# Optimization experiments

Measured on AMD Instinct MI355X. Metric: run time of the kernel, lower is better.

The kernel has to match this reference:

```python
import jax, jax.numpy as jnp
import numpy as np

N_EMBD = 768
N_HEAD = 8
B, T = 4, 2048

def setup_inputs() -> dict:
    key = jax.random.key(0)
    k1, k2, k3, k4, k5 = jax.random.split(key, 5)
    C = N_EMBD
    s = 1.0 / np.sqrt(C)
    return {
        "x": jax.random.normal(k1, (B, T, C), dtype=jnp.float32),
        "W_attn": jax.random.normal(k2, (C, 3 * C), dtype=jnp.float32) * s,
        "b_attn": jnp.zeros((3 * C,), dtype=jnp.float32),
        "W_proj": jax.random.normal(k3, (C, C), dtype=jnp.float32) * s,
        "b_proj": jnp.zeros((C,), dtype=jnp.float32),
    }

def reference(x, W_attn, b_attn, W_proj, b_proj):
    Bs, Ts, C = x.shape
    H = N_HEAD
    hs = C // H
    qkv = x @ W_attn + b_attn                      # [B,T,3C]
    q, k, v = jnp.split(qkv, 3, axis=-1)
    # reshape to [B,H,T,hs]
    q = q.reshape(Bs, Ts, H, hs).transpose(0, 2, 1, 3)
    k = k.reshape(Bs, Ts, H, hs).transpose(0, 2, 1, 3)
    v = v.reshape(Bs, Ts, H, hs).transpose(0, 2, 1, 3)
    scale = 1.0 / jnp.sqrt(jnp.float32(hs))
    att = jnp.einsum('bhid,bhjd->bhij', q, k) * scale   # [B,H,T,T]
    mask = jnp.tril(jnp.ones((Ts, Ts), dtype=bool))
    att = jnp.where(mask, att, -jnp.inf)
    m = jnp.max(att, axis=-1, keepdims=True)
    e = jnp.where(mask, jnp.exp(att - m), 0.0)
    # original kernel divides by (sum + 1e-9)
    att = e / (jnp.sum(e, axis=-1, keepdims=True) + 1e-9)
    y = jnp.einsum('bhij,bhjd->bhid', att, v)           # [B,H,T,hs]
    y = y.transpose(0, 2, 1, 3).reshape(Bs, Ts, C)
    return y @ W_proj + b_proj
```

## Files before the change

### kernel.cpp

```cpp
#include <hip/hip_runtime.h>

typedef __bf16 bf16;
typedef __attribute__((ext_vector_type(4))) __bf16 bf16x4;
typedef __attribute__((ext_vector_type(8))) __bf16 bf16x8;
typedef __attribute__((ext_vector_type(4))) float f32x4;

#define B_   4
#define T_   2048
#define C_   768
#define H_   8
#define HS_  96
#define M_   (B_ * T_)
#define QKN_ (3 * C_)

#define NEG_BIG (-1e30f)

#define KSTR 104
#define VSTR 72

__device__ __forceinline__ void gload_lds16(const bf16* g, bf16* l) {
    __builtin_amdgcn_global_load_lds(
        (const __attribute__((address_space(1))) uint32_t*)g,
        (__attribute__((address_space(3))) uint32_t*)l,
        16, 0, 0);
}

__device__ __forceinline__ bf16x8 cvt8(f32x4 v0, f32x4 v1) {
    bf16x8 o;
#pragma unroll
    for (int i = 0; i < 4; ++i) { o[i] = (bf16)v0[i]; o[4 + i] = (bf16)v1[i]; }
    return o;
}

__global__ void transpose_kernel(const float* __restrict__ W, bf16* __restrict__ Wt,
                                 int R, int Cn) {
    __shared__ bf16 tile[32][33];
    int tx = threadIdx.x, ty = threadIdx.y;
    int x  = blockIdx.x * 32 + tx;
    int y0 = blockIdx.y * 32;
#pragma unroll
    for (int j = 0; j < 32; j += 8)
        tile[ty + j][tx] = (bf16)W[(size_t)(y0 + ty + j) * Cn + x];
    __syncthreads();
    int y2 = blockIdx.x * 32;
    int x2 = y0 + tx;
#pragma unroll
    for (int j = 0; j < 32; j += 8)
        Wt[(size_t)(y2 + ty + j) * R + x2] = tile[tx][ty + j];
}

__global__ void sentinel_kernel(float* __restrict__ out, int n) {
    int i = blockIdx.x * 256 + threadIdx.x;
    if (i < n) out[i] = 12345.0f;
}

__global__ __launch_bounds__(256) void convert_bf16_kernel(const float* __restrict__ in,
                                                           bf16* __restrict__ out,
                                                           int n8) {
    int i = blockIdx.x * 256 + threadIdx.x;
    if (i >= n8) return;
    const float* p = in + (size_t)i * 8;
    f32x4 a = *(const f32x4*)p;
    f32x4 b = *(const f32x4*)(p + 4);
    *(bf16x8*)&out[(size_t)i * 8] = cvt8(a, b);
}

#define CONV_BLKS (M_ * C_ / 8 / 256)
#define TA_BX (QKN_ / 32)
#define TA_BLKS (TA_BX * (C_ / 32))
#define TP_BX (C_ / 32)
#define TP_BLKS (TP_BX * (C_ / 32))

__device__ __forceinline__ void transpose_body(bf16 (*tile)[33],
                                               const float* __restrict__ W,
                                               bf16* __restrict__ Wt,
                                               int R, int Cn, int bx, int by, int tid) {
    int tx = tid & 31, ty = tid >> 5;
    int x  = bx * 32 + tx;
    int y0 = by * 32;
#pragma unroll
    for (int j = 0; j < 32; j += 8)
        tile[ty + j][tx] = (bf16)W[(size_t)(y0 + ty + j) * Cn + x];
    __syncthreads();
    int y2 = bx * 32;
    int x2 = y0 + tx;
#pragma unroll
    for (int j = 0; j < 32; j += 8)
        Wt[(size_t)(y2 + ty + j) * R + x2] = tile[tx][ty + j];
}

__global__ __launch_bounds__(256) void prep_kernel(const float* __restrict__ x,
                                                   bf16* __restrict__ xb,
                                                   const float* __restrict__ Wa,
                                                   bf16* __restrict__ Wta,
                                                   const float* __restrict__ Wp,
                                                   bf16* __restrict__ Wtp) {
    __shared__ bf16 tile[32][33];
    int bid = blockIdx.x;
    int tid = threadIdx.x;
    if (bid < CONV_BLKS) {
        int i = bid * 256 + tid;
        const float* p = x + (size_t)i * 8;
        f32x4 a = *(const f32x4*)p;
        f32x4 b = *(const f32x4*)(p + 4);
        *(bf16x8*)&xb[(size_t)i * 8] = cvt8(a, b);
    } else if (bid < CONV_BLKS + TA_BLKS) {
        int t = bid - CONV_BLKS;
        transpose_body(tile, Wa, Wta, C_, QKN_, t % TA_BX, t / TA_BX, tid);
    } else {
        int t = bid - CONV_BLKS - TA_BLKS;
        transpose_body(tile, Wp, Wtp, C_, C_, t % TP_BX, t / TP_BX, tid);
    }
}

#define TILE_ELEMS (128 * 64)

__global__ __launch_bounds__(256) void gemm_qkv(const bf16* __restrict__ A,
                                                const bf16* __restrict__ Bt,
                                                const float* __restrict__ bias,
                                                bf16* __restrict__ Cmat,
                                                bf16* __restrict__ Vt,
                                                int M, int N, int K) {
    __shared__ bf16 lda[2 * TILE_ELEMS];
    __shared__ bf16 ldb[2 * TILE_ELEMS];
    int tid  = threadIdx.x;
    int w    = tid >> 6;
    int lane = tid & 63;
    int col  = lane & 15, quad = lane >> 4;
    int wr   = w >> 1, wc = w & 1;
    int m0   = blockIdx.y * 128, n0 = blockIdx.x * 128;

    int srow = lane >> 3;
    int scol = ((lane & 7) ^ srow) * 8;
    const bf16* gA[4]; const bf16* gB[4]; bf16* lA[4]; bf16* lB[4];
#pragma unroll
    for (int i = 0; i < 4; ++i) {
        int seg = w * 4 + i;
        int row = seg * 8 + srow;
        gA[i] = &A[(size_t)(m0 + row) * K + scol];
        gB[i] = &Bt[(size_t)(n0 + row) * K + scol];
        lA[i] = &lda[seg * 512];
        lB[i] = &ldb[seg * 512];
    }

    const f32x4 zero = {0.f, 0.f, 0.f, 0.f};
    f32x4 acc[4][4];
#pragma unroll
    for (int mr = 0; mr < 4; ++mr)
#pragma unroll
        for (int nc = 0; nc < 4; ++nc) acc[mr][nc] = zero;

#pragma unroll
    for (int i = 0; i < 4; ++i) {
        gload_lds16(gA[i], lA[i]);
        gload_lds16(gB[i], lB[i]);
    }

    int cur = 0;
    for (int k0 = 0; k0 < K; k0 += 64) {
        int nxt = cur ^ 1;
        if (k0 + 64 < K) {
#pragma unroll
            for (int i = 0; i < 4; ++i) {
                gload_lds16(gA[i] + k0 + 64, lA[i] + nxt * TILE_ELEMS);
                gload_lds16(gB[i] + k0 + 64, lB[i] + nxt * TILE_ELEMS);
            }
            asm volatile("s_waitcnt vmcnt(8)" ::: "memory");
        } else {
            asm volatile("s_waitcnt vmcnt(0)" ::: "memory");
        }
        __builtin_amdgcn_s_barrier();
        __builtin_amdgcn_sched_barrier(0);
        const bf16* la = &lda[cur * TILE_ELEMS];
        const bf16* lb = &ldb[cur * TILE_ELEMS];
#pragma unroll
        for (int ks = 0; ks < 2; ++ks) {
            bf16x8 af[4], bfr[4];
            int ca = (((ks * 4 + quad) ^ (col & 7)) * 8);
#pragma unroll
            for (int t = 0; t < 4; ++t) {
                af[t]  = *(const bf16x8*)&la[(wr * 64 + t * 16 + col) * 64 + ca];
                bfr[t] = *(const bf16x8*)&lb[(wc * 64 + t * 16 + col) * 64 + ca];
            }
#pragma unroll
            for (int mr = 0; mr < 4; ++mr)
#pragma unroll
                for (int nc = 0; nc < 4; ++nc)
                    acc[mr][nc] = __builtin_amdgcn_mfma_f32_16x16x32_bf16(
                        af[mr], bfr[nc], acc[mr][nc], 0, 0, 0);
        }
        __builtin_amdgcn_sched_barrier(0);
        __builtin_amdgcn_s_barrier();
        cur = nxt;
    }

#pragma unroll
    for (int nc = 0; nc < 4; ++nc) {
        int n = n0 + wc * 64 + nc * 16 + col;
        float bv = bias[n];
#pragma unroll
        for (int mr = 0; mr < 4; ++mr) {
#pragma unroll
            for (int r = 0; r < 4; ++r) {
                int row = m0 + wr * 64 + mr * 16 + quad * 4 + r;
                Cmat[(size_t)row * N + n] = (bf16)(acc[mr][nc][r] + bv);
            }
        }
    }
    if (n0 >= 2 * C_) {
        int batch = m0 >> 11;
        bf16* Vtb = Vt + (size_t)batch * C_ * T_;
        int t0 = (m0 & 2047) + wr * 64;
#pragma unroll
        for (int nc = 0; nc < 4; ++nc) {
            int n  = n0 + wc * 64 + nc * 16 + col;
            int vc = n - 2 * C_;
            float bv = bias[n];
#pragma unroll
            for (int mr = 0; mr < 4; ++mr) {
                int t  = t0 + mr * 16 + quad * 4;
                int tb = t & ~63;
                int a  = (t >> 2) & 15;
                int ts = tb + ((a & 7) << 3) + ((a >> 3) << 2);
                bf16x4 pk = {(bf16)(acc[mr][nc][0] + bv), (bf16)(acc[mr][nc][1] + bv),
                             (bf16)(acc[mr][nc][2] + bv), (bf16)(acc[mr][nc][3] + bv)};
                *(bf16x4*)&Vtb[(size_t)vc * T_ + ts] = pk;
            }
        }
    }
}

#define PJA_ELEMS (128 * 64)
#define PJB_ELEMS (96 * 64)
__global__ __launch_bounds__(256) void gemm_proj(const bf16* __restrict__ A,
                                                 const bf16* __restrict__ Bt,
                                                 const float* __restrict__ bias,
                                                 float* __restrict__ Cmat,
                                                 int M, int N, int K) {
    __shared__ bf16 lda[2 * PJA_ELEMS];
    __shared__ bf16 ldb[2 * PJB_ELEMS];
    int tid  = threadIdx.x;
    int w    = tid >> 6;
    int lane = tid & 63;
    int col  = lane & 15, quad = lane >> 4;
    int wr   = w >> 1, wc = w & 1;
    int m0   = blockIdx.y * 128, n0 = blockIdx.x * 96;

    int srow = lane >> 3;
    int scol = ((lane & 7) ^ srow) * 8;
    const bf16* gA[4]; bf16* lA[4];
    const bf16* gB[3]; bf16* lB[3];
#pragma unroll
    for (int i = 0; i < 4; ++i) {
        int seg = w * 4 + i;
        int row = seg * 8 + srow;
        gA[i] = &A[(size_t)(m0 + row) * K + scol];
        lA[i] = &lda[seg * 512];
    }
#pragma unroll
    for (int i = 0; i < 3; ++i) {
        int seg = w * 3 + i;
        int row = seg * 8 + srow;
        gB[i] = &Bt[(size_t)(n0 + row) * K + scol];
        lB[i] = &ldb[seg * 512];
    }

    const f32x4 zero = {0.f, 0.f, 0.f, 0.f};
    f32x4 acc[4][3];
#pragma unroll
    for (int mr = 0; mr < 4; ++mr)
#pragma unroll
        for (int nc = 0; nc < 3; ++nc) acc[mr][nc] = zero;

#pragma unroll
    for (int i = 0; i < 4; ++i) gload_lds16(gA[i], lA[i]);
#pragma unroll
    for (int i = 0; i < 3; ++i) gload_lds16(gB[i], lB[i]);

    int cur = 0;
    for (int k0 = 0; k0 < K; k0 += 64) {
        int nxt = cur ^ 1;
        if (k0 + 64 < K) {
#pragma unroll
            for (int i = 0; i < 4; ++i)
                gload_lds16(gA[i] + k0 + 64, lA[i] + nxt * PJA_ELEMS);
#pragma unroll
            for (int i = 0; i < 3; ++i)
                gload_lds16(gB[i] + k0 + 64, lB[i] + nxt * PJB_ELEMS);
            asm volatile("s_waitcnt vmcnt(7)" ::: "memory");
        } else {
            asm volatile("s_waitcnt vmcnt(0)" ::: "memory");
        }
        __builtin_amdgcn_s_barrier();
        __builtin_amdgcn_sched_barrier(0);
        const bf16* la = &lda[cur * PJA_ELEMS];
        const bf16* lb = &ldb[cur * PJB_ELEMS];
#pragma unroll
        for (int ks = 0; ks < 2; ++ks) {
            bf16x8 af[4], bfr[3];
            int ca = (((ks * 4 + quad) ^ (col & 7)) * 8);
#pragma unroll
            for (int t = 0; t < 4; ++t)
                af[t]  = *(const bf16x8*)&la[(wr * 64 + t * 16 + col) * 64 + ca];
#pragma unroll
            for (int t = 0; t < 3; ++t)
                bfr[t] = *(const bf16x8*)&lb[(wc * 48 + t * 16 + col) * 64 + ca];
#pragma unroll
            for (int mr = 0; mr < 4; ++mr)
#pragma unroll
                for (int nc = 0; nc < 3; ++nc)
                    acc[mr][nc] = __builtin_amdgcn_mfma_f32_16x16x32_bf16(
                        af[mr], bfr[nc], acc[mr][nc], 0, 0, 0);
        }
        __builtin_amdgcn_sched_barrier(0);
        __builtin_amdgcn_s_barrier();
        cur = nxt;
    }

#pragma unroll
    for (int nc = 0; nc < 3; ++nc) {
        int n = n0 + wc * 48 + nc * 16 + col;
        float bv = bias[n];
#pragma unroll
        for (int mr = 0; mr < 4; ++mr) {
#pragma unroll
            for (int r = 0; r < 4; ++r) {
                int row = m0 + wr * 64 + mr * 16 + quad * 4 + r;
                Cmat[(size_t)row * N + n] = acc[mr][nc][r] + bv;
            }
        }
    }
}

__global__ __launch_bounds__(256) void attn_kernel(const bf16* __restrict__ qkv,
                                                   const bf16* __restrict__ Vt,
                                                   bf16* __restrict__ y,
                                                   int nGroups) {
    __shared__ bf16 ldsK[64 * KSTR];
    __shared__ bf16 ldsV[96 * VSTR];
    const int bid  = blockIdx.x;
    const int qt   = 31 - bid / nGroups;
    const int g    = bid % nGroups;
    const int h    = g & 7, b = g >> 3;
    const int tid  = threadIdx.x;
    const int w    = tid >> 6, lane = tid & 63;
    const int col  = lane & 15, quad = lane >> 4;
    const float SCALE2 = 0.10206207261596577f * 1.4426950408889634f;
    const float M0 = 24.0f;
    const f32x4 zero = {0.f, 0.f, 0.f, 0.f};

    const bf16* qkvb = qkv + (size_t)b * T_ * QKN_;
    const bf16* Vtbh = Vt + (size_t)(b * H_ + h) * HS_ * T_;
    bf16* yb  = y + (size_t)b * T_ * C_;

    const int rbase = qt * 64 + w * 16;

    bf16x8 qf[3];
#pragma unroll
    for (int c = 0; c < 3; ++c)
        qf[c] = *(const bf16x8*)&qkvb[(size_t)(rbase + col) * QKN_ + h * HS_ + c * 32 + quad * 8];

    const bf16* pK[3]; const bf16* pV[3];
    bf16 *dK[3], *dV[3];
#pragma unroll
    for (int i = 0; i < 3; ++i) {
        int chunk = i * 256 + tid;
        int rK = chunk / 12, cK = chunk - rK * 12;
        pK[i] = qkvb + (size_t)rK * QKN_ + C_ + h * HS_ + cK * 8;
        dK[i] = &ldsK[rK * KSTR + cK * 8];
        int rV = chunk >> 3, cV = chunk & 7;
        pV[i] = Vtbh + (size_t)rV * T_ + cV * 8;
        dV[i] = &ldsV[rV * VSTR + cV * 8];
    }

    f32x4 o[6];
#pragma unroll
    for (int n2 = 0; n2 < 6; ++n2) o[n2] = zero;
    f32x4 lsum4 = zero;

    bf16x8 kreg[3], vreg[3];
#pragma unroll
    for (int i = 0; i < 3; ++i) {
        kreg[i] = *(const bf16x8*)pK[i];
        vreg[i] = *(const bf16x8*)pV[i];
        pK[i] += (size_t)64 * QKN_;
        pV[i] += 64;
    }

    const int njt = qt + 1;
    for (int jt = 0; jt < njt; ++jt) {
        int jb = jt * 64;
        __syncthreads();
#pragma unroll
        for (int i = 0; i < 3; ++i) {
            *(bf16x8*)dK[i] = kreg[i];
            *(bf16x8*)dV[i] = vreg[i];
        }
        __syncthreads();
        if (jt + 1 < njt) {
#pragma unroll
            for (int i = 0; i < 3; ++i) {
                kreg[i] = *(const bf16x8*)pK[i];
                vreg[i] = *(const bf16x8*)pV[i];
                pK[i] += (size_t)64 * QKN_;
                pV[i] += 64;
            }
        }

        f32x4 st[4];
        __builtin_amdgcn_s_setprio(1);
#pragma unroll
        for (int nb = 0; nb < 4; ++nb) {
            st[nb] = zero;
#pragma unroll
            for (int c = 0; c < 3; ++c) {
                bf16x8 kf = *(const bf16x8*)&ldsK[(nb * 16 + col) * KSTR + c * 32 + quad * 8];
                st[nb] = __builtin_amdgcn_mfma_f32_16x16x32_bf16(
                    kf, qf[c], st[nb], 0, 0, 0);
            }
        }
        __builtin_amdgcn_s_setprio(0);

        if (jt == njt - 1) {
#pragma unroll
            for (int nb = 0; nb < 4; ++nb)
#pragma unroll
                for (int r = 0; r < 4; ++r) {
                    int jg = jb + nb * 16 + quad * 4 + r;
                    st[nb][r] = (jg <= rbase + col) ? fmaf(st[nb][r], SCALE2, -M0)
                                                    : NEG_BIG;
                }
        } else {
#pragma unroll
            for (int nb = 0; nb < 4; ++nb)
#pragma unroll
                for (int r = 0; r < 4; ++r)
                    st[nb][r] = fmaf(st[nb][r], SCALE2, -M0);
        }

#pragma unroll
        for (int nb = 0; nb < 4; ++nb) {
#pragma unroll
            for (int r = 0; r < 4; ++r)
                st[nb][r] = exp2f(st[nb][r]);
            lsum4 += st[nb];
        }

        bf16x8 palo, pahi;
#pragma unroll
        for (int r = 0; r < 4; ++r) {
            palo[r]     = (bf16)st[0][r];
            palo[4 + r] = (bf16)st[2][r];
            pahi[r]     = (bf16)st[1][r];
            pahi[4 + r] = (bf16)st[3][r];
        }

        __builtin_amdgcn_s_setprio(1);
#pragma unroll
        for (int n2 = 0; n2 < 6; ++n2) {
            const bf16* vrow = &ldsV[(n2 * 16 + col) * VSTR];
            bf16x8 vlo = *(const bf16x8*)&vrow[quad * 8];
            bf16x8 vhi = *(const bf16x8*)&vrow[32 + quad * 8];
            o[n2] = __builtin_amdgcn_mfma_f32_16x16x32_bf16(vlo, palo, o[n2], 0, 0, 0);
            o[n2] = __builtin_amdgcn_mfma_f32_16x16x32_bf16(vhi, pahi, o[n2], 0, 0, 0);
        }
        __builtin_amdgcn_s_setprio(0);
    }

    float lsum = (lsum4[0] + lsum4[1]) + (lsum4[2] + lsum4[3]);
    lsum += __shfl_xor(lsum, 16, 64);
    lsum += __shfl_xor(lsum, 32, 64);
    float linv = 1.0f / lsum;
#pragma unroll
    for (int n2 = 0; n2 < 6; ++n2) {
        bf16x4 pk = {(bf16)(o[n2][0] * linv), (bf16)(o[n2][1] * linv),
                     (bf16)(o[n2][2] * linv), (bf16)(o[n2][3] * linv)};
        *(bf16x4*)&yb[(size_t)(rbase + col) * C_ + h * HS_ + n2 * 16 + quad * 4] = pk;
    }
}

extern "C" void kernel_launch(void* const* d_in, const int* in_sizes, int n_in,
                              void* d_out, int out_size, void* d_ws, size_t ws_size,
                              hipStream_t stream) {
    (void)in_sizes; (void)n_in;
    const float* x      = (const float*)d_in[0];
    const float* W_attn = (const float*)d_in[1];
    const float* b_attn = (const float*)d_in[2];
    const float* W_proj = (const float*)d_in[3];
    const float* b_proj = (const float*)d_in[4];
    float* out = (float*)d_out;

    size_t e_wta = (size_t)QKN_ * C_;
    size_t e_wtp = (size_t)C_ * C_;
    size_t a_qkv = e_wta + e_wtp;
    size_t a_vt  = a_qkv + (size_t)M_ * QKN_;
    size_t a_yb  = a_vt + (size_t)M_ * C_;
    size_t needA = (a_yb + (size_t)M_ * C_) * sizeof(bf16);
    size_t b_qkv = e_wta + e_wtp;
    size_t b_vt  = b_qkv + (size_t)T_ * QKN_;
    size_t b_yb  = b_vt + (size_t)T_ * C_;
    size_t needB = (b_yb + (size_t)T_ * C_) * sizeof(bf16);

    if (ws_size >= needA) {
        bf16* Wt_attn = (bf16*)d_ws;
        bf16* Wt_proj = (bf16*)d_ws + e_wta;
        bf16* qkv     = (bf16*)d_ws + a_qkv;
        bf16* Vt      = (bf16*)d_ws + a_vt;
        bf16* yb      = (bf16*)d_ws + a_yb;
        bf16* xb      = yb;
        prep_kernel<<<dim3(CONV_BLKS + TA_BLKS + TP_BLKS), 256, 0, stream>>>(
            x, xb, W_attn, Wt_attn, W_proj, Wt_proj);
        gemm_qkv<<<dim3(QKN_ / 128, M_ / 128), 256, 0, stream>>>(
            xb, Wt_attn, b_attn, qkv, Vt, M_, QKN_, C_);
        attn_kernel<<<dim3(32 * H_ * B_), 256, 0, stream>>>(qkv, Vt, yb, H_ * B_);
        gemm_proj<<<dim3(C_ / 96, M_ / 128), 256, 0, stream>>>(
            yb, Wt_proj, b_proj, out, M_, C_, C_);
    } else if (ws_size >= needB) {
        bf16* Wt_attn = (bf16*)d_ws;
        bf16* Wt_proj = (bf16*)d_ws + e_wta;
        bf16* qkv     = (bf16*)d_ws + b_qkv;
        bf16* Vt      = (bf16*)d_ws + b_vt;
        bf16* yb      = (bf16*)d_ws + b_yb;
        bf16* xb      = yb;
        transpose_kernel<<<dim3(QKN_ / 32, C_ / 32), dim3(32, 8), 0, stream>>>(W_attn, Wt_attn, C_, QKN_);
        transpose_kernel<<<dim3(C_ / 32, C_ / 32), dim3(32, 8), 0, stream>>>(W_proj, Wt_proj, C_, C_);
        for (int b = 0; b < B_; ++b) {
            const float* xf = x + (size_t)b * T_ * C_;
            float* outb     = out + (size_t)b * T_ * C_;
            convert_bf16_kernel<<<dim3(T_ * C_ / 8 / 256), 256, 0, stream>>>(xf, xb, T_ * C_ / 8);
            gemm_qkv<<<dim3(QKN_ / 128, T_ / 128), 256, 0, stream>>>(
                xb, Wt_attn, b_attn, qkv, Vt, T_, QKN_, C_);
            attn_kernel<<<dim3(32 * H_), 256, 0, stream>>>(qkv, Vt, yb, H_);
            gemm_proj<<<dim3(C_ / 96, T_ / 128), 256, 0, stream>>>(
                yb, Wt_proj, b_proj, outb, T_, C_, C_);
        }
    } else {
        sentinel_kernel<<<(out_size + 255) / 256, 256, 0, stream>>>(out, out_size);
    }
}
```

Baseline: 201.8 us.

## Split long causal attention query tiles across two blocks with a combine pass

```diff
diff --git a/kernel.cpp b/kernel.cpp
--- a/kernel.cpp
+++ b/kernel.cpp
@@ -332,6 +332,196 @@
     }
 }
 
+__global__ __launch_bounds__(256) void attn_split_kernel(const bf16* __restrict__ qkv,
+                                                         const bf16* __restrict__ Vt,
+                                                         bf16* __restrict__ y,
+                                                         float* __restrict__ Osl,
+                                                         float* __restrict__ Lsl,
+                                                         int nGroups) {
+    __shared__ bf16 ldsK[64 * KSTR];
+    __shared__ bf16 ldsV[96 * VSTR];
+    const int bid  = blockIdx.x;
+    const int job  = bid / nGroups;
+    const int g    = bid % nGroups;
+    int qt, jt0, jt1;
+    bool split;
+    if (job < 32) {
+        qt = 31 - (job >> 1);
+        split = true;
+        int njt = qt + 1, mid = njt >> 1;
+        if ((job & 1) == 0) { jt0 = 0;   jt1 = mid; }
+        else                { jt0 = mid; jt1 = njt; }
+    } else {
+        qt = 47 - job;
+        split = false; jt0 = 0; jt1 = qt + 1;
+    }
+    const int h    = g & 7, b = g >> 3;
+    const int tid  = threadIdx.x;
+    const int w    = tid >> 6, lane = tid & 63;
+    const int col  = lane & 15, quad = lane >> 4;
+    const float SCALE2 = 0.10206207261596577f * 1.4426950408889634f;
+    const float M0 = 24.0f;
+    const f32x4 zero = {0.f, 0.f, 0.f, 0.f};
+
+    const bf16* qkvb = qkv + (size_t)b * T_ * QKN_;
+    const bf16* Vtbh = Vt + (size_t)(b * H_ + h) * HS_ * T_;
+    bf16* yb  = y + (size_t)b * T_ * C_;
+
+    const int rbase = qt * 64 + w * 16;
+
+    bf16x8 qf[3];
+#pragma unroll
+    for (int c = 0; c < 3; ++c)
+        qf[c] = *(const bf16x8*)&qkvb[(size_t)(rbase + col) * QKN_ + h * HS_ + c * 32 + quad * 8];
+
+    const bf16* pK[3]; const bf16* pV[3];
+    bf16 *dK[3], *dV[3];
+#pragma unroll
+    for (int i = 0; i < 3; ++i) {
+        int chunk = i * 256 + tid;
+        int rK = chunk / 12, cK = chunk - rK * 12;
+        pK[i] = qkvb + (size_t)(jt0 * 64 + rK) * QKN_ + C_ + h * HS_ + cK * 8;
+        dK[i] = &ldsK[rK * KSTR + cK * 8];
+        int rV = chunk >> 3, cV = chunk & 7;
+        pV[i] = Vtbh + (size_t)rV * T_ + jt0 * 64 + cV * 8;
+        dV[i] = &ldsV[rV * VSTR + cV * 8];
+    }
+
+    f32x4 o[6];
+#pragma unroll
+    for (int n2 = 0; n2 < 6; ++n2) o[n2] = zero;
+    f32x4 lsum4 = zero;
+
+    bf16x8 kreg[3], vreg[3];
+#pragma unroll
+    for (int i = 0; i < 3; ++i) {
+        kreg[i] = *(const bf16x8*)pK[i];
+        vreg[i] = *(const bf16x8*)pV[i];
+        pK[i] += (size_t)64 * QKN_;
+        pV[i] += 64;
+    }
+
+    for (int jt = jt0; jt < jt1; ++jt) {
+        int jb = jt * 64;
+        __syncthreads();
+#pragma unroll
+        for (int i = 0; i < 3; ++i) {
+            *(bf16x8*)dK[i] = kreg[i];
+            *(bf16x8*)dV[i] = vreg[i];
+        }
+        __syncthreads();
+        if (jt + 1 < jt1) {
+#pragma unroll
+            for (int i = 0; i < 3; ++i) {
+                kreg[i] = *(const bf16x8*)pK[i];
+                vreg[i] = *(const bf16x8*)pV[i];
+                pK[i] += (size_t)64 * QKN_;
+                pV[i] += 64;
+            }
+        }
+
+        f32x4 st[4];
+        __builtin_amdgcn_s_setprio(1);
+#pragma unroll
+        for (int nb = 0; nb < 4; ++nb) {
+            st[nb] = zero;
+#pragma unroll
+            for (int c = 0; c < 3; ++c) {
+                bf16x8 kf = *(const bf16x8*)&ldsK[(nb * 16 + col) * KSTR + c * 32 + quad * 8];
+                st[nb] = __builtin_amdgcn_mfma_f32_16x16x32_bf16(
+                    kf, qf[c], st[nb], 0, 0, 0);
+            }
+        }
+        __builtin_amdgcn_s_setprio(0);
+
+        if (jt == qt) {
+#pragma unroll
+            for (int nb = 0; nb < 4; ++nb)
+#pragma unroll
+                for (int r = 0; r < 4; ++r) {
+                    int jg = jb + nb * 16 + quad * 4 + r;
+                    st[nb][r] = (jg <= rbase + col) ? fmaf(st[nb][r], SCALE2, -M0)
+                                                    : NEG_BIG;
+                }
+        } else {
+#pragma unroll
+            for (int nb = 0; nb < 4; ++nb)
+#pragma unroll
+                for (int r = 0; r < 4; ++r)
+                    st[nb][r] = fmaf(st[nb][r], SCALE2, -M0);
+        }
+
+#pragma unroll
+        for (int nb = 0; nb < 4; ++nb) {
+#pragma unroll
+            for (int r = 0; r < 4; ++r)
+                st[nb][r] = exp2f(st[nb][r]);
+            lsum4 += st[nb];
+        }
+
+        bf16x8 palo, pahi;
+#pragma unroll
+        for (int r = 0; r < 4; ++r) {
+            palo[r]     = (bf16)st[0][r];
+            palo[4 + r] = (bf16)st[2][r];
+            pahi[r]     = (bf16)st[1][r];
+            pahi[4 + r] = (bf16)st[3][r];
+        }
+
+        __builtin_amdgcn_s_setprio(1);
+#pragma unroll
+        for (int n2 = 0; n2 < 6; ++n2) {
+            const bf16* vrow = &ldsV[(n2 * 16 + col) * VSTR];
+            bf16x8 vlo = *(const bf16x8*)&vrow[quad * 8];
+            bf16x8 vhi = *(const bf16x8*)&vrow[32 + quad * 8];
+            o[n2] = __builtin_amdgcn_mfma_f32_16x16x32_bf16(vlo, palo, o[n2], 0, 0, 0);
+            o[n2] = __builtin_amdgcn_mfma_f32_16x16x32_bf16(vhi, pahi, o[n2], 0, 0, 0);
+        }
+        __builtin_amdgcn_s_setprio(0);
+    }
+
+    float lsum = (lsum4[0] + lsum4[1]) + (lsum4[2] + lsum4[3]);
+    lsum += __shfl_xor(lsum, 16, 64);
+    lsum += __shfl_xor(lsum, 32, 64);
+    if (split) {
+        int half = job & 1;
+        int rowl = rbase + col - 1024;
+        float* Ob = Osl + ((size_t)(half * B_ + b)) * 1024 * C_;
+        float* Lb = Lsl + ((size_t)(half * B_ + b)) * H_ * 1024 + (size_t)h * 1024;
+        if (quad == 0) Lb[rowl] = lsum;
+#pragma unroll
+        for (int n2 = 0; n2 < 6; ++n2)
+            *(f32x4*)&Ob[(size_t)rowl * C_ + h * HS_ + n2 * 16 + quad * 4] = o[n2];
+    } else {
+        float linv = 1.0f / lsum;
+#pragma unroll
+        for (int n2 = 0; n2 < 6; ++n2) {
+            bf16x4 pk = {(bf16)(o[n2][0] * linv), (bf16)(o[n2][1] * linv),
+                         (bf16)(o[n2][2] * linv), (bf16)(o[n2][3] * linv)};
+            *(bf16x4*)&yb[(size_t)(rbase + col) * C_ + h * HS_ + n2 * 16 + quad * 4] = pk;
+        }
+    }
+}
+
+__global__ __launch_bounds__(256) void attn_combine_kernel(const float* __restrict__ Osl,
+                                                           const float* __restrict__ Lsl,
+                                                           bf16* __restrict__ y) {
+    int i = blockIdx.x * 256 + threadIdx.x;
+    int e = i * 4;
+    int r = e / C_, c = e - r * C_;
+    int b = r >> 10, rl = r & 1023;
+    int h = c / HS_;
+    const size_t OS = (size_t)B_ * 1024 * C_;
+    const size_t LS = (size_t)B_ * H_ * 1024;
+    f32x4 o0 = *(const f32x4*)&Osl[e];
+    f32x4 o1 = *(const f32x4*)&Osl[OS + e];
+    size_t li = ((size_t)b * H_ + h) * 1024 + rl;
+    float inv = 1.0f / (Lsl[li] + Lsl[LS + li]);
+    bf16x4 pk = {(bf16)((o0[0] + o1[0]) * inv), (bf16)((o0[1] + o1[1]) * inv),
+                 (bf16)((o0[2] + o1[2]) * inv), (bf16)((o0[3] + o1[3]) * inv)};
+    *(bf16x4*)&y[(size_t)b * T_ * C_ + (size_t)(1024 + rl) * C_ + c] = pk;
+}
+
 __global__ __launch_bounds__(256) void attn_kernel(const bf16* __restrict__ qkv,
                                                    const bf16* __restrict__ Vt,
                                                    bf16* __restrict__ y,
@@ -496,6 +686,9 @@
     size_t a_vt  = a_qkv + (size_t)M_ * QKN_;
     size_t a_yb  = a_vt + (size_t)M_ * C_;
     size_t needA = (a_yb + (size_t)M_ * C_) * sizeof(bf16);
+    size_t oslF  = (size_t)2 * B_ * 1024 * C_;
+    size_t lslF  = (size_t)2 * B_ * H_ * 1024;
+    size_t needS = needA + (oslF + lslF) * sizeof(float);
     size_t b_qkv = e_wta + e_wtp;
     size_t b_vt  = b_qkv + (size_t)T_ * QKN_;
     size_t b_yb  = b_vt + (size_t)T_ * C_;
@@ -512,7 +705,16 @@
             x, xb, W_attn, Wt_attn, W_proj, Wt_proj);
         gemm_qkv<<<dim3(QKN_ / 128, M_ / 128), 256, 0, stream>>>(
             xb, Wt_attn, b_attn, qkv, Vt, M_, QKN_, C_);
-        attn_kernel<<<dim3(32 * H_ * B_), 256, 0, stream>>>(qkv, Vt, yb, H_ * B_);
+        if (ws_size >= needS) {
+            float* Osl = (float*)((char*)d_ws + needA);
+            float* Lsl = Osl + oslF;
+            attn_split_kernel<<<dim3(48 * H_ * B_), 256, 0, stream>>>(
+                qkv, Vt, yb, Osl, Lsl, H_ * B_);
+            attn_combine_kernel<<<dim3(B_ * 1024 * C_ / 4 / 256), 256, 0, stream>>>(
+                Osl, Lsl, yb);
+        } else {
+            attn_kernel<<<dim3(32 * H_ * B_), 256, 0, stream>>>(qkv, Vt, yb, H_ * B_);
+        }
         gemm_proj<<<dim3(C_ / 96, M_ / 128), 256, 0, stream>>>(
             yb, Wt_proj, b_proj, out, M_, C_, C_);
     } else if (ws_size >= needB) {
```

Result: slower. 218.0 us (+8.0%).
